# Performance work log

Hardware: AMD Instinct MI355X
Metric: run time of the kernel (lower is better)

## Reference

```python
import jax, jax.numpy as jnp
import numpy as np

BITW = 1
BITA = 3
BATCH = 8192
IN_CH = 4096
N_UNITS = 4096


def _quantize(x, k):
    # DoReFa uniform quantizer with straight-through estimator (round -> identity grad)
    n = float(2 ** k - 1)
    return x + jax.lax.stop_gradient(jnp.round(x * n) / n - x)


def _cabs(x):
    # clip magnitude to [0, 1]
    return jnp.minimum(1.0, jnp.abs(x))


def quantize_active(x, bitA):
    if bitA == 32:
        return x
    return _quantize(x, bitA)


def quantize_weight(w, bitW):
    if bitW == 32:
        return w
    if bitW == 1:
        # binary weights scaled by mean |w| (E is treated as constant)
        E = jax.lax.stop_gradient(jnp.mean(jnp.abs(w)))
        y = w / E
        # sign with straight-through gradient
        return (y + jax.lax.stop_gradient(jnp.sign(y) - y)) * E
    t = jnp.tanh(w)
    t = t / jnp.max(jnp.abs(t)) * 0.5 + 0.5
    return 2.0 * _quantize(t, bitW) - 1.0


def setup_inputs() -> dict:
    key = jax.random.key(0)
    k1, k2 = jax.random.split(key)
    inputs = jax.random.normal(k1, (BATCH, IN_CH), dtype=jnp.float32)
    # truncated_normal(stddev=0.1) init approximated with normal * 0.1
    W = jax.random.normal(k2, (IN_CH, N_UNITS), dtype=jnp.float32) * 0.1
    b = jnp.zeros((N_UNITS,), dtype=jnp.float32)
    return {"inputs": inputs, "W": W, "b": b}


def reference(inputs, W, b):
    q_in = quantize_active(_cabs(inputs), BITA)   # [B, IN] in {0..1} grid of 2^bitA-1 levels
    q_W = quantize_weight(W, BITW)                # [IN, OUT] binary (+-E)
    out = jnp.matmul(q_in, q_W) + b               # [B, OUT]
    return out
```

## Files before the change

kernel.cpp:

```cpp
#include <hip/hip_runtime.h>


static constexpr int BATCH  = 8192;
static constexpr int IN_CH  = 4096;
static constexpr int NUNITS = 4096;
static constexpr int TPB    = 256;

typedef int v4i __attribute__((ext_vector_type(4)));

static constexpr size_t A8_OFF   = 0;
static constexpr size_t A8_BYTES = (size_t)BATCH * IN_CH;
static constexpr size_t BT_OFF   = A8_OFF + A8_BYTES;
static constexpr size_t BT_BYTES = (size_t)NUNITS * IN_CH;
static constexpr int    NPART    = 4096;
static constexpr size_t PART_OFF = BT_OFF + BT_BYTES;
static constexpr size_t SCALE_OFF= PART_OFF + NPART * sizeof(float);

__global__ __launch_bounds__(TPB) void k_scale(const float* __restrict__ partials,
                                               float* __restrict__ scale) {
    __shared__ float red[TPB];
    float s = 0.f;
    for (int i = threadIdx.x; i < NPART; i += TPB) s += partials[i];
    red[threadIdx.x] = s;
    __syncthreads();
    for (int off = TPB / 2; off > 0; off >>= 1) {
        if ((int)threadIdx.x < off) red[threadIdx.x] += red[threadIdx.x + off];
        __syncthreads();
    }
    if (threadIdx.x == 0) {
        float E = red[0] / (float)((size_t)IN_CH * NUNITS);
        *scale = E / 7.0f;
    }
}

__device__ __forceinline__ unsigned int q4(float4 v) {
    unsigned int b0 = (unsigned int)(int)rintf(fminf(1.0f, fabsf(v.x)) * 7.0f);
    unsigned int b1 = (unsigned int)(int)rintf(fminf(1.0f, fabsf(v.y)) * 7.0f);
    unsigned int b2 = (unsigned int)(int)rintf(fminf(1.0f, fabsf(v.z)) * 7.0f);
    unsigned int b3 = (unsigned int)(int)rintf(fminf(1.0f, fabsf(v.w)) * 7.0f);
    return b0 | (b1 << 8) | (b2 << 16) | (b3 << 24);
}

__global__ __launch_bounds__(TPB) void k_quant_a(const float4* __restrict__ x4,
                                                 uint4* __restrict__ a16) {
    const size_t t = (size_t)blockIdx.x * TPB + threadIdx.x;
    uint4 o;
    o.x = q4(x4[t * 4 + 0]);
    o.y = q4(x4[t * 4 + 1]);
    o.z = q4(x4[t * 4 + 2]);
    o.w = q4(x4[t * 4 + 3]);
    a16[t] = o;
}

__global__ __launch_bounds__(TPB) void k_signT(const float* __restrict__ W,
                                               char* __restrict__ bt,
                                               float* __restrict__ partials) {
    __shared__ char tile[64][68];
    __shared__ float red[TPB];
    const int bk = blockIdx.x & 63;
    const int bn = blockIdx.x >> 6;
    const int t  = threadIdx.x;
    const int c  = t & 63;
    const int r0 = t >> 6;
    float asum = 0.f;
#pragma unroll
    for (int i = 0; i < 16; ++i) {
        int r = i * 4 + r0;
        float w = W[(size_t)(bk * 64 + r) * NUNITS + bn * 64 + c];
        asum += fabsf(w);
        tile[c][r] = (w > 0.f) ? 1 : ((w < 0.f) ? -1 : 0);
    }
    __syncthreads();
    const int n  = t >> 2;
    const int kk = (t & 3) * 16;
    char o[16];
#pragma unroll
    for (int j = 0; j < 16; ++j) o[j] = tile[n][kk + j];
    *(uint4*)(bt + (size_t)(bn * 64 + n) * IN_CH + bk * 64 + kk) = *(const uint4*)o;

    red[t] = asum;
    __syncthreads();
    for (int off = TPB / 2; off > 0; off >>= 1) {
        if (t < off) red[t] += red[t + off];
        __syncthreads();
    }
    if (t == 0) partials[blockIdx.x] = red[0];
}

__device__ __forceinline__ void gload_lds16(const void* g, void* l) {
    __builtin_amdgcn_global_load_lds((const __attribute__((address_space(1))) void*)g,
                                     (__attribute__((address_space(3))) void*)l,
                                     16, 0, 0);
}

#define VMCNT4   asm volatile("s_waitcnt vmcnt(4)" ::: "memory")
#define VMCNT0   asm volatile("s_waitcnt vmcnt(0)" ::: "memory")
#define LGKM0    asm volatile("s_waitcnt lgkmcnt(0)" ::: "memory")
#define SCHEDB   __builtin_amdgcn_sched_barrier(0)
#define BARRIER  __builtin_amdgcn_s_barrier()
#define PRIO1    __builtin_amdgcn_s_setprio(1)
#define PRIO0    __builtin_amdgcn_s_setprio(0)

static constexpr int NT = IN_CH / 64;

__global__ __launch_bounds__(512, 2) void k_gemm(const char* __restrict__ A8,
                                                 const char* __restrict__ BT,
                                                 const float* __restrict__ scale_p,
                                                 const float* __restrict__ bias,
                                                 float* __restrict__ out) {
    __shared__ char Ms[3][32768];

    const int t    = threadIdx.x;
    const int bid  = blockIdx.x;
    const int swzb = (bid & 7) * 64 + (bid >> 3);
    const int bRow = swzb >> 4;
    const int bCol = swzb & 15;
    const int lane = t & 63;
    const int wid  = t >> 6;
    const int wm   = wid >> 2;
    const int wn   = wid & 3;
    const int lr   = lane & 15;
    const int lk4  = lane >> 4;

    const size_t aBase = (size_t)(bRow * 256) * IN_CH;
    const size_t bBase = (size_t)(bCol * 256) * IN_CH;

    const int aswz = ((lk4 ^ (lr & 7)) << 4);
    const int bswz = aswz ^ 64;

    const int srow  = t >> 3;
    const int pslot = t & 7;
    const int lslot = pslot ^ (srow & 7);
    const char* mbase = (lslot < 4) ? (A8 + aBase) : (BT + bBase);
    const char* sbase = mbase + (size_t)srow * IN_CH + (size_t)((lslot & 3) << 4);

    v4i acc[8][4] = {};

#define STAGE4(kt, STG)                                                         \
    _Pragma("unroll") for (int h = 0; h < 4; ++h)                               \
        gload_lds16(sbase + (size_t)h * 64 * IN_CH + (size_t)(kt) * 64,         \
                    (STG) + h * 8192 + wid * 1024)

#define TILE(kt, CUR, STG, LAST)                                                \
    do {                                                                        \
        SCHEDB; LGKM0;                                                         \
        if (LAST) { VMCNT0; } else { VMCNT4; }                                  \
        BARRIER; SCHEDB;                                                        \
        if ((kt) + 2 < NT) { STAGE4((kt) + 2, STG); }                           \
        v4i a_[8], b_[4];                                                       \
        _Pragma("unroll") for (int m = 0; m < 8; ++m)                           \
            a_[m] = *(const v4i*)((CUR) + (wm * 128 + m * 16 + lr) * 128 + aswz); \
        _Pragma("unroll") for (int n = 0; n < 4; ++n)                           \
            b_[n] = *(const v4i*)((CUR) + (wn * 64 + n * 16 + lr) * 128 + bswz); \
        PRIO1;                                                                  \
        _Pragma("unroll") for (int m = 0; m < 8; ++m)                           \
            _Pragma("unroll") for (int n = 0; n < 4; ++n)                       \
                acc[m][n] = __builtin_amdgcn_mfma_i32_16x16x64_i8(              \
                    a_[m], b_[n], acc[m][n], 0, 0, 0);                          \
        PRIO0;                                                                  \
    } while (0)

    char* B0 = (char*)Ms[0];
    char* B1 = (char*)Ms[1];
    char* B2 = (char*)Ms[2];

    STAGE4(0, B0);
    STAGE4(1, B1);

    for (int T = 0; T < NT - 1; T += 3) {
        TILE(T,     B0, B2, false);
        TILE(T + 1, B1, B0, false);
        TILE(T + 2, B2, B1, false);
    }
    TILE(NT - 1, B0, B2, true);

    const float scale = *scale_p;
    const int orow0 = bRow * 256 + wm * 128;
    const int ocol0 = bCol * 256 + wn * 64;
#pragma unroll
    for (int m = 0; m < 8; ++m) {
#pragma unroll
        for (int n = 0; n < 4; ++n) {
            const int col = ocol0 + n * 16 + lr;
            const float bb = bias[col];
            const int rbase = orow0 + m * 16 + lk4 * 4;
#pragma unroll
            for (int j = 0; j < 4; ++j)
                out[(size_t)(rbase + j) * NUNITS + col] = scale * (float)acc[m][n][j] + bb;
        }
    }
#undef STAGE4
#undef TILE
}

extern "C" void kernel_launch(void* const* d_in, const int* in_sizes, int n_in,
                              void* d_out, int out_size, void* d_ws, size_t ws_size,
                              hipStream_t stream) {
    const float* x  = (const float*)d_in[0];
    const float* W  = (const float*)d_in[1];
    const float* b  = (const float*)d_in[2];
    float* out      = (float*)d_out;

    char*  ws       = (char*)d_ws;
    char*  A8       = ws + A8_OFF;
    char*  BT       = ws + BT_OFF;
    float* partials = (float*)(ws + PART_OFF);
    float* scale    = (float*)(ws + SCALE_OFF);

    k_signT<<<(IN_CH / 64) * (NUNITS / 64), TPB, 0, stream>>>(W, BT, partials);
    k_scale<<<1, TPB, 0, stream>>>(partials, scale);
    k_quant_a<<<(BATCH * (IN_CH / 16)) / TPB, TPB, 0, stream>>>((const float4*)x, (uint4*)A8);
    k_gemm<<<(BATCH / 256) * (NUNITS / 256), 512, 0, stream>>>(A8, BT, scale, b, out);
}
```

Measured before the change: 181.9 us.

## Deepen GEMM LDS pipeline to five buffers and interleave LDS reads with MFMA

```diff
diff --git a/kernel.cpp b/kernel.cpp
--- a/kernel.cpp
+++ b/kernel.cpp
@@ -93,13 +93,13 @@
                                      16, 0, 0);
 }
 
+#define VMCNT8   asm volatile("s_waitcnt vmcnt(8)" ::: "memory")
 #define VMCNT4   asm volatile("s_waitcnt vmcnt(4)" ::: "memory")
 #define VMCNT0   asm volatile("s_waitcnt vmcnt(0)" ::: "memory")
-#define LGKM0    asm volatile("s_waitcnt lgkmcnt(0)" ::: "memory")
-#define SCHEDB   __builtin_amdgcn_sched_barrier(0)
 #define BARRIER  __builtin_amdgcn_s_barrier()
 #define PRIO1    __builtin_amdgcn_s_setprio(1)
 #define PRIO0    __builtin_amdgcn_s_setprio(0)
+#define SGB(mask, n) __builtin_amdgcn_sched_group_barrier((mask), (n), 0)
 
 static constexpr int NT = IN_CH / 64;
 
@@ -108,7 +108,7 @@
                                                  const float* __restrict__ scale_p,
                                                  const float* __restrict__ bias,
                                                  float* __restrict__ out) {
-    __shared__ char Ms[3][32768];
+    __shared__ char Ms[5][32768];
 
     const int t    = threadIdx.x;
     const int bid  = blockIdx.x;
@@ -141,38 +141,61 @@
         gload_lds16(sbase + (size_t)h * 64 * IN_CH + (size_t)(kt) * 64,         \
                     (STG) + h * 8192 + wid * 1024)
 
-#define TILE(kt, CUR, STG, LAST)                                                \
-    do {                                                                        \
-        SCHEDB; LGKM0;                                                         \
-        if (LAST) { VMCNT0; } else { VMCNT4; }                                  \
-        BARRIER; SCHEDB;                                                        \
-        if ((kt) + 2 < NT) { STAGE4((kt) + 2, STG); }                           \
-        v4i a_[8], b_[4];                                                       \
-        _Pragma("unroll") for (int m = 0; m < 8; ++m)                           \
-            a_[m] = *(const v4i*)((CUR) + (wm * 128 + m * 16 + lr) * 128 + aswz); \
-        _Pragma("unroll") for (int n = 0; n < 4; ++n)                           \
+#define RD_A(i, CUR) a_[i] = *(const v4i*)((CUR) + (wm * 128 + (i) * 16 + lr) * 128 + aswz)
+#define MFMA8(m0)                                                                \
+    _Pragma("unroll") for (int n = 0; n < 4; ++n)                                \
+        acc[m0][n] = __builtin_amdgcn_mfma_i32_16x16x64_i8(a_[m0], b_[n], acc[m0][n], 0, 0, 0); \
+    _Pragma("unroll") for (int n = 0; n < 4; ++n)                                \
+        acc[(m0)+1][n] = __builtin_amdgcn_mfma_i32_16x16x64_i8(a_[(m0)+1], b_[n], acc[(m0)+1][n], 0, 0, 0)
+
+#define TILE(CUR, DOSTAGE, KSTG, STG, WAIT)                                      \
+    do {                                                                         \
+        if (DOSTAGE) { STAGE4(KSTG, STG); }                                      \
+        v4i a_[8], b_[4];                                                        \
+        _Pragma("unroll") for (int n = 0; n < 4; ++n)                            \
             b_[n] = *(const v4i*)((CUR) + (wn * 64 + n * 16 + lr) * 128 + bswz); \
-        PRIO1;                                                                  \
-        _Pragma("unroll") for (int m = 0; m < 8; ++m)                           \
-            _Pragma("unroll") for (int n = 0; n < 4; ++n)                       \
-                acc[m][n] = __builtin_amdgcn_mfma_i32_16x16x64_i8(              \
-                    a_[m], b_[n], acc[m][n], 0, 0, 0);                          \
-        PRIO0;                                                                  \
+        RD_A(0, CUR); RD_A(1, CUR);                                              \
+        PRIO1;                                                                   \
+        MFMA8(0);                                                                \
+        RD_A(2, CUR); RD_A(3, CUR);                                              \
+        MFMA8(2);                                                                \
+        RD_A(4, CUR); RD_A(5, CUR);                                              \
+        MFMA8(4);                                                                \
+        RD_A(6, CUR); RD_A(7, CUR);                                              \
+        MFMA8(6);                                                                \
+        PRIO0;                                                                   \
+        if (DOSTAGE) { SGB(0x10, 4); }                                           \
+        SGB(0x100, 6); SGB(0x8, 16);                                             \
+        SGB(0x100, 2); SGB(0x8, 16);                                             \
+        SGB(0x100, 2); SGB(0x8, 16);                                             \
+        SGB(0x100, 2); SGB(0x8, 16);                                             \
+        WAIT;                                                                    \
+        BARRIER;                                                                 \
     } while (0)
 
     char* B0 = (char*)Ms[0];
     char* B1 = (char*)Ms[1];
     char* B2 = (char*)Ms[2];
+    char* B3 = (char*)Ms[3];
+    char* B4 = (char*)Ms[4];
 
     STAGE4(0, B0);
     STAGE4(1, B1);
-
-    for (int T = 0; T < NT - 1; T += 3) {
-        TILE(T,     B0, B2, false);
-        TILE(T + 1, B1, B0, false);
-        TILE(T + 2, B2, B1, false);
-    }
-    TILE(NT - 1, B0, B2, true);
+    STAGE4(2, B2);
+    VMCNT8;
+    BARRIER;
+
+    for (int T = 0; T < 60; T += 5) {
+        TILE(B0, true, T + 3, B3, VMCNT8);
+        TILE(B1, true, T + 4, B4, VMCNT8);
+        TILE(B2, true, T + 5, B0, VMCNT8);
+        TILE(B3, true, T + 6, B1, VMCNT8);
+        TILE(B4, true, T + 7, B2, VMCNT8);
+    }
+    TILE(B0, true, 63, B3, VMCNT8);
+    TILE(B1, false, 0, B0, VMCNT4);
+    TILE(B2, false, 0, B0, VMCNT0);
+    TILE(B3, false, 0, B0, (void)0);
 
     const float scale = *scale_p;
     const int orow0 = bRow * 256 + wm * 128;
@@ -191,6 +214,8 @@
     }
 #undef STAGE4
 #undef TILE
+#undef RD_A
+#undef MFMA8
 }
 
 extern "C" void kernel_launch(void* const* d_in, const int* in_sizes, int n_in,
```

Result: no change. 182.5 us (+0.3%).

## Load B fragments directly to registers and deepen A LDS pipeline with scheduled MFMA

Applied to the files above, without the earlier changes.

```diff
diff --git a/kernel.cpp b/kernel.cpp
--- a/kernel.cpp
+++ b/kernel.cpp
@@ -93,13 +93,12 @@
                                      16, 0, 0);
 }
 
-#define VMCNT4   asm volatile("s_waitcnt vmcnt(4)" ::: "memory")
+#define VMCNT2   asm volatile("s_waitcnt vmcnt(2)" ::: "memory")
 #define VMCNT0   asm volatile("s_waitcnt vmcnt(0)" ::: "memory")
-#define LGKM0    asm volatile("s_waitcnt lgkmcnt(0)" ::: "memory")
-#define SCHEDB   __builtin_amdgcn_sched_barrier(0)
 #define BARRIER  __builtin_amdgcn_s_barrier()
 #define PRIO1    __builtin_amdgcn_s_setprio(1)
 #define PRIO0    __builtin_amdgcn_s_setprio(0)
+#define SGB(mask, n) __builtin_amdgcn_sched_group_barrier((mask), (n), 0)
 
 static constexpr int NT = IN_CH / 64;
 
@@ -108,7 +107,7 @@
                                                  const float* __restrict__ scale_p,
                                                  const float* __restrict__ bias,
                                                  float* __restrict__ out) {
-    __shared__ char Ms[3][32768];
+    __shared__ char Aflat[4 * 16384];
 
     const int t    = threadIdx.x;
     const int bid  = blockIdx.x;
@@ -123,56 +122,77 @@
     const int lk4  = lane >> 4;
 
     const size_t aBase = (size_t)(bRow * 256) * IN_CH;
-    const size_t bBase = (size_t)(bCol * 256) * IN_CH;
-
-    const int aswz = ((lk4 ^ (lr & 7)) << 4);
-    const int bswz = aswz ^ 64;
-
-    const int srow  = t >> 3;
-    const int pslot = t & 7;
-    const int lslot = pslot ^ (srow & 7);
-    const char* mbase = (lslot < 4) ? (A8 + aBase) : (BT + bBase);
-    const char* sbase = mbase + (size_t)srow * IN_CH + (size_t)((lslot & 3) << 4);
+
+    const int aoff = (((wm * 4 + lk4) ^ (lr & 7)) << 4);
+#define RD(buf, i) (*(const v4i*)((buf) + (((i) * 16 + lr) * 128) + aoff))
+
+    const int s_log   = (t & 7) ^ ((t >> 3) & 7);
+    const int rowbase = ((s_log >> 2) << 7) + (t >> 3);
+    const char* sA    = A8 + aBase + (size_t)rowbase * IN_CH + ((s_log & 3) << 4);
+
+    const char* bptr = BT + ((size_t)(bCol * 256 + wn * 64 + lr)) * IN_CH + (lk4 << 4);
 
     v4i acc[8][4] = {};
-
-#define STAGE4(kt, STG)                                                         \
-    _Pragma("unroll") for (int h = 0; h < 4; ++h)                               \
-        gload_lds16(sbase + (size_t)h * 64 * IN_CH + (size_t)(kt) * 64,         \
-                    (STG) + h * 8192 + wid * 1024)
-
-#define TILE(kt, CUR, STG, LAST)                                                \
-    do {                                                                        \
-        SCHEDB; LGKM0;                                                         \
-        if (LAST) { VMCNT0; } else { VMCNT4; }                                  \
-        BARRIER; SCHEDB;                                                        \
-        if ((kt) + 2 < NT) { STAGE4((kt) + 2, STG); }                           \
-        v4i a_[8], b_[4];                                                       \
-        _Pragma("unroll") for (int m = 0; m < 8; ++m)                           \
-            a_[m] = *(const v4i*)((CUR) + (wm * 128 + m * 16 + lr) * 128 + aswz); \
-        _Pragma("unroll") for (int n = 0; n < 4; ++n)                           \
-            b_[n] = *(const v4i*)((CUR) + (wn * 64 + n * 16 + lr) * 128 + bswz); \
-        PRIO1;                                                                  \
-        _Pragma("unroll") for (int m = 0; m < 8; ++m)                           \
-            _Pragma("unroll") for (int n = 0; n < 4; ++n)                       \
-                acc[m][n] = __builtin_amdgcn_mfma_i32_16x16x64_i8(              \
-                    a_[m], b_[n], acc[m][n], 0, 0, 0);                          \
-        PRIO0;                                                                  \
-    } while (0)
-
-    char* B0 = (char*)Ms[0];
-    char* B1 = (char*)Ms[1];
-    char* B2 = (char*)Ms[2];
-
-    STAGE4(0, B0);
-    STAGE4(1, B1);
-
-    for (int T = 0; T < NT - 1; T += 3) {
-        TILE(T,     B0, B2, false);
-        TILE(T + 1, B1, B0, false);
-        TILE(T + 2, B2, B1, false);
-    }
-    TILE(NT - 1, B0, B2, true);
+    v4i bA[4], bB[4];
+    v4i ap0, ap1;
+
+#define MFMA8(x, y, m0, B)                                                       \
+    PRIO1;                                                                       \
+    _Pragma("unroll") for (int n = 0; n < 4; ++n) {                              \
+        acc[(m0)][n]     = __builtin_amdgcn_mfma_i32_16x16x64_i8((x), B[n], acc[(m0)][n], 0, 0, 0);     \
+        acc[(m0) + 1][n] = __builtin_amdgcn_mfma_i32_16x16x64_i8((y), B[n], acc[(m0) + 1][n], 0, 0, 0); \
+    }                                                                            \
+    PRIO0
+
+#define STAGEA(kt)                                                               \
+    _Pragma("unroll") for (int h = 0; h < 2; ++h)                                \
+        gload_lds16(sA + (size_t)h * 64 * IN_CH + (size_t)(kt) * 64,             \
+                    Aflat + (((kt) & 3) << 14) + h * 8192 + t * 16)
+
+#define LOADB(BN, kt)                                                            \
+    _Pragma("unroll") for (int n = 0; n < 4; ++n)                                \
+        BN[n] = *(const v4i*)(bptr + (size_t)n * 16 * IN_CH + (size_t)(kt) * 64)
+
+#define BODY(T, BC, BN, DOB, DOSTG, DOPF, GATE, DOSGB)                           \
+    {                                                                            \
+        const char* cur = Aflat + (((T) & 3) << 14);                             \
+        if (DOB) { LOADB(BN, (T) + 1); }                                         \
+        if (DOSTG) { STAGEA((T) + 3); }                                          \
+        v4i a2 = RD(cur, 2), a3 = RD(cur, 3);                                    \
+        MFMA8(ap0, ap1, 0, BC);                                                  \
+        v4i a4 = RD(cur, 4), a5 = RD(cur, 5);                                    \
+        MFMA8(a2, a3, 2, BC);                                                    \
+        v4i a6 = RD(cur, 6), a7 = RD(cur, 7);                                    \
+        MFMA8(a4, a5, 4, BC);                                                    \
+        if (DOPF) { const char* nb = Aflat + ((((T) + 1) & 3) << 14);            \
+                    ap0 = RD(nb, 0); ap1 = RD(nb, 1); }                          \
+        MFMA8(a6, a7, 6, BC);                                                    \
+        if (DOSGB) { SGB(0x10, 6);                                               \
+                     SGB(0x100, 2); SGB(0x8, 8); SGB(0x100, 2); SGB(0x8, 8);     \
+                     SGB(0x100, 2); SGB(0x8, 8); SGB(0x100, 2); SGB(0x8, 8); }   \
+        GATE;                                                                    \
+        BARRIER;                                                                 \
+    }
+
+    STAGEA(0);
+    STAGEA(1);
+    STAGEA(2);
+    LOADB(bA, 0);
+    VMCNT0;
+    BARRIER;
+    {
+        const char* b0 = Aflat;
+        ap0 = RD(b0, 0); ap1 = RD(b0, 1);
+    }
+
+    for (int T = 0; T < 60; T += 2) {
+        BODY(T,     bA, bB, 1, 1, 1, VMCNT2, 1);
+        BODY(T + 1, bB, bA, 1, 1, 1, VMCNT2, 1);
+    }
+    BODY(60, bA, bB, 1, 1, 1, VMCNT2, 1);
+    BODY(61, bB, bA, 1, 0, 1, VMCNT0, 0);
+    BODY(62, bA, bB, 1, 0, 1, VMCNT0, 0);
+    BODY(63, bB, bA, 0, 0, 0, (void)0, 0);
 
     const float scale = *scale_p;
     const int orow0 = bRow * 256 + wm * 128;
@@ -189,8 +209,11 @@
                 out[(size_t)(rbase + j) * NUNITS + col] = scale * (float)acc[m][n][j] + bb;
         }
     }
-#undef STAGE4
-#undef TILE
+#undef BODY
+#undef LOADB
+#undef STAGEA
+#undef MFMA8
+#undef RD
 }
 
 extern "C" void kernel_launch(void* const* d_in, const int* in_sizes, int n_in,
```

Result: slower. 260.5 us (+43.2%).

## Shrink GEMM tile to 128x128 with 256 threads and fuse scale reduction

Applied to the files above, without the earlier changes.

```diff
diff --git a/kernel.cpp b/kernel.cpp
--- a/kernel.cpp
+++ b/kernel.cpp
@@ -15,42 +15,6 @@
 static constexpr int    NPART    = 4096;
 static constexpr size_t PART_OFF = BT_OFF + BT_BYTES;
 static constexpr size_t SCALE_OFF= PART_OFF + NPART * sizeof(float);
-
-__global__ __launch_bounds__(TPB) void k_scale(const float* __restrict__ partials,
-                                               float* __restrict__ scale) {
-    __shared__ float red[TPB];
-    float s = 0.f;
-    for (int i = threadIdx.x; i < NPART; i += TPB) s += partials[i];
-    red[threadIdx.x] = s;
-    __syncthreads();
-    for (int off = TPB / 2; off > 0; off >>= 1) {
-        if ((int)threadIdx.x < off) red[threadIdx.x] += red[threadIdx.x + off];
-        __syncthreads();
-    }
-    if (threadIdx.x == 0) {
-        float E = red[0] / (float)((size_t)IN_CH * NUNITS);
-        *scale = E / 7.0f;
-    }
-}
-
-__device__ __forceinline__ unsigned int q4(float4 v) {
-    unsigned int b0 = (unsigned int)(int)rintf(fminf(1.0f, fabsf(v.x)) * 7.0f);
-    unsigned int b1 = (unsigned int)(int)rintf(fminf(1.0f, fabsf(v.y)) * 7.0f);
-    unsigned int b2 = (unsigned int)(int)rintf(fminf(1.0f, fabsf(v.z)) * 7.0f);
-    unsigned int b3 = (unsigned int)(int)rintf(fminf(1.0f, fabsf(v.w)) * 7.0f);
-    return b0 | (b1 << 8) | (b2 << 16) | (b3 << 24);
-}
-
-__global__ __launch_bounds__(TPB) void k_quant_a(const float4* __restrict__ x4,
-                                                 uint4* __restrict__ a16) {
-    const size_t t = (size_t)blockIdx.x * TPB + threadIdx.x;
-    uint4 o;
-    o.x = q4(x4[t * 4 + 0]);
-    o.y = q4(x4[t * 4 + 1]);
-    o.z = q4(x4[t * 4 + 2]);
-    o.w = q4(x4[t * 4 + 3]);
-    a16[t] = o;
-}
 
 __global__ __launch_bounds__(TPB) void k_signT(const float* __restrict__ W,
                                                char* __restrict__ bt,
@@ -87,6 +51,42 @@
     if (t == 0) partials[blockIdx.x] = red[0];
 }
 
+__device__ __forceinline__ unsigned int q4(float4 v) {
+    unsigned int b0 = (unsigned int)(int)rintf(fminf(1.0f, fabsf(v.x)) * 7.0f);
+    unsigned int b1 = (unsigned int)(int)rintf(fminf(1.0f, fabsf(v.y)) * 7.0f);
+    unsigned int b2 = (unsigned int)(int)rintf(fminf(1.0f, fabsf(v.z)) * 7.0f);
+    unsigned int b3 = (unsigned int)(int)rintf(fminf(1.0f, fabsf(v.w)) * 7.0f);
+    return b0 | (b1 << 8) | (b2 << 16) | (b3 << 24);
+}
+
+__global__ __launch_bounds__(TPB) void k_quant_a(const float4* __restrict__ x4,
+                                                 uint4* __restrict__ a16,
+                                                 const float* __restrict__ partials,
+                                                 float* __restrict__ scale) {
+    if (blockIdx.x == 0) {
+        __shared__ float red[TPB];
+        float s = 0.f;
+        for (int i = threadIdx.x; i < NPART; i += TPB) s += partials[i];
+        red[threadIdx.x] = s;
+        __syncthreads();
+        for (int off = TPB / 2; off > 0; off >>= 1) {
+            if ((int)threadIdx.x < off) red[threadIdx.x] += red[threadIdx.x + off];
+            __syncthreads();
+        }
+        if (threadIdx.x == 0) {
+            float E = red[0] / (float)((size_t)IN_CH * NUNITS);
+            *scale = E / 7.0f;
+        }
+    }
+    const size_t t = (size_t)blockIdx.x * TPB + threadIdx.x;
+    uint4 o;
+    o.x = q4(x4[t * 4 + 0]);
+    o.y = q4(x4[t * 4 + 1]);
+    o.z = q4(x4[t * 4 + 2]);
+    o.w = q4(x4[t * 4 + 3]);
+    a16[t] = o;
+}
+
 __device__ __forceinline__ void gload_lds16(const void* g, void* l) {
     __builtin_amdgcn_global_load_lds((const __attribute__((address_space(1))) void*)g,
                                      (__attribute__((address_space(3))) void*)l,
@@ -103,61 +103,58 @@
 
 static constexpr int NT = IN_CH / 64;
 
-__global__ __launch_bounds__(512, 2) void k_gemm(const char* __restrict__ A8,
+__global__ __launch_bounds__(256, 3) void k_gemm(const char* __restrict__ A8,
                                                  const char* __restrict__ BT,
                                                  const float* __restrict__ scale_p,
                                                  const float* __restrict__ bias,
                                                  float* __restrict__ out) {
-    __shared__ char Ms[3][32768];
+    __shared__ char Ms[3][16384];
 
     const int t    = threadIdx.x;
     const int bid  = blockIdx.x;
-    const int swzb = (bid & 7) * 64 + (bid >> 3);
-    const int bRow = swzb >> 4;
-    const int bCol = swzb & 15;
+    const int swzb = (bid & 7) * 256 + (bid >> 3);
+    const int bRow = swzb >> 5;
+    const int bCol = swzb & 31;
     const int lane = t & 63;
     const int wid  = t >> 6;
-    const int wm   = wid >> 2;
-    const int wn   = wid & 3;
+    const int wr   = wid >> 1;
+    const int wc   = wid & 1;
     const int lr   = lane & 15;
     const int lk4  = lane >> 4;
 
-    const size_t aBase = (size_t)(bRow * 256) * IN_CH;
-    const size_t bBase = (size_t)(bCol * 256) * IN_CH;
-
-    const int aswz = ((lk4 ^ (lr & 7)) << 4);
-    const int bswz = aswz ^ 64;
-
-    const int srow  = t >> 3;
-    const int pslot = t & 7;
-    const int lslot = pslot ^ (srow & 7);
-    const char* mbase = (lslot < 4) ? (A8 + aBase) : (BT + bBase);
-    const char* sbase = mbase + (size_t)srow * IN_CH + (size_t)((lslot & 3) << 4);
-
-    v4i acc[8][4] = {};
-
-#define STAGE4(kt, STG)                                                         \
-    _Pragma("unroll") for (int h = 0; h < 4; ++h)                               \
-        gload_lds16(sbase + (size_t)h * 64 * IN_CH + (size_t)(kt) * 64,         \
-                    (STG) + h * 8192 + wid * 1024)
-
-#define TILE(kt, CUR, STG, LAST)                                                \
-    do {                                                                        \
-        SCHEDB; LGKM0;                                                         \
-        if (LAST) { VMCNT0; } else { VMCNT4; }                                  \
-        BARRIER; SCHEDB;                                                        \
-        if ((kt) + 2 < NT) { STAGE4((kt) + 2, STG); }                           \
-        v4i a_[8], b_[4];                                                       \
-        _Pragma("unroll") for (int m = 0; m < 8; ++m)                           \
-            a_[m] = *(const v4i*)((CUR) + (wm * 128 + m * 16 + lr) * 128 + aswz); \
-        _Pragma("unroll") for (int n = 0; n < 4; ++n)                           \
-            b_[n] = *(const v4i*)((CUR) + (wn * 64 + n * 16 + lr) * 128 + bswz); \
-        PRIO1;                                                                  \
-        _Pragma("unroll") for (int m = 0; m < 8; ++m)                           \
-            _Pragma("unroll") for (int n = 0; n < 4; ++n)                       \
-                acc[m][n] = __builtin_amdgcn_mfma_i32_16x16x64_i8(              \
-                    a_[m], b_[n], acc[m][n], 0, 0, 0);                          \
-        PRIO0;                                                                  \
+    const int aoff = ((lk4 ^ (lr & 7)) << 4);
+    const int boff = aoff ^ 64;
+
+    const int lslot = (t & 7) ^ ((t >> 3) & 7);
+    const char* mbase = (lslot < 4)
+        ? (A8 + (size_t)(bRow * 128) * IN_CH)
+        : (BT + (size_t)(bCol * 128) * IN_CH);
+    const char* sbase = mbase + (size_t)(t >> 3) * IN_CH + ((lslot & 3) << 4);
+
+    v4i acc[4][4] = {};
+
+#define STAGE4(kt, STG)                                                          \
+    _Pragma("unroll") for (int h = 0; h < 4; ++h)                                \
+        gload_lds16(sbase + (size_t)h * 32 * IN_CH + (size_t)(kt) * 64,          \
+                    (STG) + h * 4096 + t * 16)
+
+#define TILE(kt, CUR, STG, LAST)                                                 \
+    do {                                                                         \
+        SCHEDB; LGKM0;                                                           \
+        if (LAST) { VMCNT0; } else { VMCNT4; }                                   \
+        BARRIER; SCHEDB;                                                         \
+        if ((kt) + 2 < NT) { STAGE4((kt) + 2, STG); }                            \
+        v4i a_[4], b_[4];                                                        \
+        _Pragma("unroll") for (int m = 0; m < 4; ++m)                            \
+            a_[m] = *(const v4i*)((CUR) + (wr * 64 + m * 16 + lr) * 128 + aoff); \
+        _Pragma("unroll") for (int n = 0; n < 4; ++n)                            \
+            b_[n] = *(const v4i*)((CUR) + (wc * 64 + n * 16 + lr) * 128 + boff); \
+        PRIO1;                                                                   \
+        _Pragma("unroll") for (int m = 0; m < 4; ++m)                            \
+            _Pragma("unroll") for (int n = 0; n < 4; ++n)                        \
+                acc[m][n] = __builtin_amdgcn_mfma_i32_16x16x64_i8(               \
+                    a_[m], b_[n], acc[m][n], 0, 0, 0);                           \
+        PRIO0;                                                                   \
     } while (0)
 
     char* B0 = (char*)Ms[0];
@@ -175,10 +172,10 @@
     TILE(NT - 1, B0, B2, true);
 
     const float scale = *scale_p;
-    const int orow0 = bRow * 256 + wm * 128;
-    const int ocol0 = bCol * 256 + wn * 64;
-#pragma unroll
-    for (int m = 0; m < 8; ++m) {
+    const int orow0 = bRow * 128 + wr * 64;
+    const int ocol0 = bCol * 128 + wc * 64;
+#pragma unroll
+    for (int m = 0; m < 4; ++m) {
 #pragma unroll
         for (int n = 0; n < 4; ++n) {
             const int col = ocol0 + n * 16 + lr;
@@ -208,7 +205,7 @@
     float* scale    = (float*)(ws + SCALE_OFF);
 
     k_signT<<<(IN_CH / 64) * (NUNITS / 64), TPB, 0, stream>>>(W, BT, partials);
-    k_scale<<<1, TPB, 0, stream>>>(partials, scale);
-    k_quant_a<<<(BATCH * (IN_CH / 16)) / TPB, TPB, 0, stream>>>((const float4*)x, (uint4*)A8);
-    k_gemm<<<(BATCH / 256) * (NUNITS / 256), 512, 0, stream>>>(A8, BT, scale, b, out);
-}
+    k_quant_a<<<(BATCH * (IN_CH / 16)) / TPB, TPB, 0, stream>>>((const float4*)x, (uint4*)A8,
+                                                                partials, scale);
+    k_gemm<<<(BATCH / 128) * (NUNITS / 128), TPB, 0, stream>>>(A8, BT, scale, b, out);
+}
```

After: 236.1 us. 29.8% more time.
